# Kernel tuning notes

Hardware: AMD Instinct MI355X
Metric: run time of the kernel (lower is better)

## Reference

```python
import jax, jax.numpy as jnp
import numpy as np

HIDDEN = 32
ODE_H = 0.1      # rk4 fixed step size (torchdiffeq options step_size=0.1)
ODE_STEPS = 10   # integrate t in [0, 1]


def gcn_conv(x, W, b, edge_index, n):
    """PyG GCNConv: symmetric norm with self-loops; x' = D^-1/2 (A+I) D^-1/2 (x W) + b."""
    h = x @ W                                  # [n, out]
    src, dst = edge_index[0], edge_index[1]
    deg = jnp.ones((n,), h.dtype).at[dst].add(1.0)   # +1 for self-loop
    dinv = jax.lax.rsqrt(deg)
    coef = (dinv[src] * dinv[dst])[:, None]
    agg = jnp.zeros_like(h).at[dst].add(h[src] * coef)
    agg = agg + h * (dinv * dinv)[:, None]     # self-loop term
    return agg + b


def ode_rk4(x0, edge_index, Wg, bg, wt, n):
    """RK4 integration of psi(t,x)=relu(GCN(x)) * sigmoid(t * wt) from t=0 to 1."""
    def f(t, x):
        gate = jax.nn.sigmoid(t * wt)          # [hidden], Linear(1,h,no bias).sigmoid()
        return jax.nn.relu(gcn_conv(x, Wg, bg, edge_index, n)) * gate

    h = ODE_H
    def step(x, t):
        k1 = f(t, x)
        k2 = f(t + h * 0.5, x + (h * 0.5) * k1)
        k3 = f(t + h * 0.5, x + (h * 0.5) * k2)
        k4 = f(t + h, x + h * k3)
        return x + (h / 6.0) * (k1 + 2.0 * k2 + 2.0 * k3 + k4), None

    ts = jnp.arange(ODE_STEPS, dtype=x0.dtype) * h
    xf, _ = jax.lax.scan(step, x0, ts)
    return xf


def setup_inputs() -> dict:
    key = jax.random.key(0)
    ks = jax.random.split(key, 16)
    N, IN, H = 100000, 128, HIDDEN
    E, DE = 1600000, 800000

    inp = {
        "H_t": jax.random.normal(ks[0], (N, IN), jnp.float32),
        "A_pos_t": jax.random.randint(ks[1], (2, E), 0, N),
        "A_neg_t": jax.random.randint(ks[2], (2, E), 0, N),
        "dA_pos": jax.random.randint(ks[3], (2, DE), 0, N),
        "dA_neg": jax.random.randint(ks[4], (2, DE), 0, N),
        # init GCN
        "W_init": jax.random.normal(ks[5], (IN, H), jnp.float32) / np.sqrt(IN),
        "b_init": jnp.zeros((H,), jnp.float32),
        # pos ODE func
        "W_pos": jax.random.normal(ks[6], (H, H), jnp.float32) / np.sqrt(H),
        "b_pos": jnp.zeros((H,), jnp.float32),
        "wt_pos": jax.random.normal(ks[7], (H,), jnp.float32),
        # neg ODE func
        "W_neg": jax.random.normal(ks[8], (H, H), jnp.float32) / np.sqrt(H),
        "b_neg": jnp.zeros((H,), jnp.float32),
        "wt_neg": jax.random.normal(ks[9], (H,), jnp.float32),
        # combine + layernorm
        "W_comb": jax.random.normal(ks[10], (2 * H, H), jnp.float32) / np.sqrt(2 * H),
        "b_comb": jnp.zeros((H,), jnp.float32),
        "ln_g": jnp.ones((H,), jnp.float32),
        "ln_b": jnp.zeros((H,), jnp.float32),
    }
    return inp


def reference(H_t, A_pos_t, A_neg_t, dA_pos, dA_neg,
              W_init, b_init, W_pos, b_pos, wt_pos,
              W_neg, b_neg, wt_neg, W_comb, b_comb, ln_g, ln_b):
    n = H_t.shape[0]
    edges_all = jnp.concatenate([A_pos_t, A_neg_t], axis=1)
    H = jax.nn.relu(gcn_conv(H_t, W_init, b_init, edges_all, n))   # [n, hidden]
    Z_pos = ode_rk4(H, dA_pos, W_pos, b_pos, wt_pos, n)
    Z_neg = ode_rk4(H, dA_neg, W_neg, b_neg, wt_neg, n)
    Z = jnp.concatenate([Z_pos, Z_neg], axis=-1) @ W_comb + b_comb # [n, hidden]
    mu = jnp.mean(Z, axis=-1, keepdims=True)
    var = jnp.var(Z, axis=-1, keepdims=True)
    return (Z - mu) * jax.lax.rsqrt(var + 1e-5) * ln_g + ln_b
```

## Files before the change

kernel.cpp:

```cpp
#include <hip/hip_runtime.h>
#include <math.h>


#define TPB 256
#define SCAN_T 1024

typedef _Float16 h8 __attribute__((ext_vector_type(8)));
typedef float f8 __attribute__((ext_vector_type(8)));


struct SegG { const int* src; const int* dst; int n; int goff; };
struct FSeg { const int* src; const int* dst; int n; const int* offs; int* cur; };

__global__ __launch_bounds__(TPB) void count_mm(
        SegG s0, SegG s1, SegG s2, SegG s3, int* __restrict__ cnt3,
        unsigned short* __restrict__ rank,
        const float* __restrict__ x, const float* __restrict__ W,
        _Float16* __restrict__ hs, int N, int cntB, int mmB) {
    __shared__ float Ws[128][32];
    __shared__ float xs[8][128];

    int g5 = blockIdx.x / 5, r5 = blockIdx.x % 5;
    if (r5 < 3) {
        int cb = g5 * 3 + r5;
        if (cb >= cntB) return;
        int i = cb * TPB + threadIdx.x;
        SegG s; int e;
        if (i < s0.n) { s = s0; e = i; }
        else if (i < s0.n + s1.n) { s = s1; e = i - s0.n; }
        else if (i < s0.n + s1.n + s2.n) { s = s2; e = i - s0.n - s1.n; }
        else if (i < s0.n + s1.n + s2.n + s3.n) { s = s3; e = i - s0.n - s1.n - s2.n; }
        else return;
        int r = atomicAdd(&cnt3[s.goff + s.dst[e]], 1);
        if (rank) rank[i] = (unsigned short)r;
    } else {
        int mb = g5 * 2 + (r5 - 3);
        if (mb >= mmB) return;
        int tid = threadIdx.x;
        for (int i = tid; i < 128 * 32; i += TPB) Ws[i >> 5][i & 31] = W[i];
        int base = mb * 8;
        for (int i = tid; i < 8 * 128; i += TPB) {
            int idx = base * 128 + i;
            xs[i >> 7][i & 127] = (idx < N * 128) ? x[idx] : 0.0f;
        }
        __syncthreads();
        int row = tid >> 5, c = tid & 31;
        int gr = base + row;
        float acc = 0.0f;
#pragma unroll
        for (int k = 0; k < 128; ++k) acc += xs[row][k] * Ws[k][c];
        if (gr < N) hs[gr * 32 + c] = (_Float16)acc;
    }
}

__global__ void fill4_rank(SegG s0, SegG s1, SegG s2, SegG s3,
                           const int* __restrict__ offs3,
                           const unsigned short* __restrict__ rank,
                           int* __restrict__ csr) {
    int i = blockIdx.x * blockDim.x + threadIdx.x;
    SegG s; int e;
    if (i < s0.n) { s = s0; e = i; }
    else if (i < s0.n + s1.n) { s = s1; e = i - s0.n; }
    else if (i < s0.n + s1.n + s2.n) { s = s2; e = i - s0.n - s1.n; }
    else if (i < s0.n + s1.n + s2.n + s3.n) { s = s3; e = i - s0.n - s1.n - s2.n; }
    else return;
    csr[offs3[s.goff + s.dst[e]] + (int)rank[i]] = s.src[e];
}

__global__ void fill4(FSeg s0, FSeg s1, FSeg s2, FSeg s3, int* __restrict__ csr) {
    int i = blockIdx.x * blockDim.x + threadIdx.x;
    FSeg s; int e;
    if (i < s0.n) { s = s0; e = i; }
    else if (i < s0.n + s1.n) { s = s1; e = i - s0.n; }
    else if (i < s0.n + s1.n + s2.n) { s = s2; e = i - s0.n - s1.n; }
    else if (i < s0.n + s1.n + s2.n + s3.n) { s = s3; e = i - s0.n - s1.n - s2.n; }
    else return;
    int d = s.dst[e];
    int pos = s.offs[d] + atomicAdd(&s.cur[d], 1);
    csr[pos] = s.src[e];
}

__global__ void scan_block(const int* __restrict__ in, int n, int* __restrict__ out,
                           int* __restrict__ bsums, float* __restrict__ dinv) {
    __shared__ int sh[SCAN_T];
    int tx = threadIdx.x;
    int g = blockIdx.x * SCAN_T + tx;
    int v = (g < n) ? in[g] : 0;
    if (g < n) dinv[g] = rsqrtf(1.0f + (float)v);
    sh[tx] = v;
    __syncthreads();
    for (int off = 1; off < SCAN_T; off <<= 1) {
        int t = (tx >= off) ? sh[tx - off] : 0;
        __syncthreads();
        sh[tx] += t;
        __syncthreads();
    }
    if (g < n) out[g] = sh[tx] - v;
    if (tx == SCAN_T - 1) bsums[blockIdx.x] = sh[tx];
}

__global__ void scan_sums(int* __restrict__ bsums, int nb) {
    __shared__ int sh[SCAN_T];
    int tx = threadIdx.x;
    int v = (tx < nb) ? bsums[tx] : 0;
    sh[tx] = v;
    __syncthreads();
    for (int off = 1; off < SCAN_T; off <<= 1) {
        int t = (tx >= off) ? sh[tx - off] : 0;
        __syncthreads();
        sh[tx] += t;
        __syncthreads();
    }
    if (tx < nb) bsums[tx] = sh[tx] - v;
}

__global__ void scan_add(int* __restrict__ offs, const int* __restrict__ bsums, int n, int total) {
    int g = blockIdx.x * blockDim.x + threadIdx.x;
    if (g < n) offs[g] += bsums[g >> 10];
    if (g == 0) offs[n] = total;
}


__global__ void mm32_kernel(const float* __restrict__ x, const float* __restrict__ W,
                            const float* __restrict__ dinv, _Float16* __restrict__ hs, int N) {
    __shared__ float Ws[32][32];
    __shared__ float xs[8][32];
    int tid = threadIdx.x;
    for (int i = tid; i < 32 * 32; i += TPB) Ws[i >> 5][i & 31] = W[i];
    int base = blockIdx.x * 8;
    {
        int idx = base * 32 + tid;
        xs[tid >> 5][tid & 31] = (idx < N * 32) ? x[idx] : 0.0f;
    }
    __syncthreads();
    int row = tid >> 5, c = tid & 31;
    int gr = base + row;
    float acc = 0.0f;
#pragma unroll
    for (int k = 0; k < 32; ++k) acc += xs[row][k] * Ws[k][c];
    if (gr < N) hs[gr * 32 + c] = (_Float16)(acc * dinv[gr]);
}


struct Job {
    const int* offs; const int* csr;
    const _Float16* hs_in; _Float16* hs_out;
    const float* dinv; const float* dinv_next;
    const float* bias; const float* wt;
    _Float16* ksum; float* x;
    const float* W;
    const float* sdinv;
};

__global__ __launch_bounds__(TPB) void agg_stage(Job jp, Job jn, int nbg, float t,
                                                 int stage, int do_mm, int split,
                                                 float* __restrict__ x2, int N) {
    __shared__ float Ws[32][32];
    __shared__ float xts[64][36];
    __shared__ int soffs[65];

    bool isP; int bid;
    if (split) {
        int xcd = blockIdx.x & 7;
        isP = xcd < 4;
        bid = ((int)blockIdx.x >> 3) * 4 + (xcd & 3);
        if (bid >= nbg) return;
    } else {
        isP = (int)blockIdx.x < nbg;
        bid = isP ? blockIdx.x : (blockIdx.x - nbg);
    }
    const Job& J = isP ? jp : jn;
    int nbase = bid * 64;
    int tid = threadIdx.x;
    int lnode = tid >> 2, q = tid & 3;
    int node = nbase + lnode;
    bool valid = node < N;

    if (do_mm) {
        for (int i = tid; i < 32 * 32; i += TPB) Ws[i >> 5][i & 31] = J.W[i];
    }
    if (tid < 65) {
        int ix = nbase + tid; if (ix > N) ix = N;
        soffs[tid] = J.offs[ix];
    }
    __syncthreads();

    f8 xrow;
#pragma unroll
    for (int j = 0; j < 8; ++j) xrow[j] = 0.f;

    if (valid) {
        const h8* hsv = (const h8*)J.hs_in;
        const int* __restrict__ csr = J.csr;
        int r0 = soffs[lnode], r1 = soffs[lnode + 1];
        f8 acc;
        if (J.sdinv) {
            const float* __restrict__ sd = J.sdinv;
            acc = __builtin_convertvector(hsv[node * 4 + q], f8) * sd[node];
            int i = r0;
            for (; i + 4 <= r1; i += 4) {
                int e0 = csr[i], e1 = csr[i + 1], e2 = csr[i + 2], e3 = csr[i + 3];
                float d0 = sd[e0], d1 = sd[e1], d2 = sd[e2], d3 = sd[e3];
                h8 v0 = hsv[e0 * 4 + q];
                h8 v1 = hsv[e1 * 4 + q];
                h8 v2 = hsv[e2 * 4 + q];
                h8 v3 = hsv[e3 * 4 + q];
                acc += __builtin_convertvector(v0, f8) * d0
                     + __builtin_convertvector(v1, f8) * d1
                     + __builtin_convertvector(v2, f8) * d2
                     + __builtin_convertvector(v3, f8) * d3;
            }
            for (; i < r1; ++i) {
                int e = csr[i];
                acc += __builtin_convertvector(hsv[e * 4 + q], f8) * sd[e];
            }
        } else {
            acc = __builtin_convertvector(hsv[node * 4 + q], f8);
            int i = r0;
            for (; i + 4 <= r1; i += 4) {
                int e0 = csr[i], e1 = csr[i + 1], e2 = csr[i + 2], e3 = csr[i + 3];
                h8 v0 = hsv[e0 * 4 + q];
                h8 v1 = hsv[e1 * 4 + q];
                h8 v2 = hsv[e2 * 4 + q];
                h8 v3 = hsv[e3 * 4 + q];
                acc += (__builtin_convertvector(v0, f8) + __builtin_convertvector(v1, f8))
                     + (__builtin_convertvector(v2, f8) + __builtin_convertvector(v3, f8));
            }
            for (; i < r1; ++i)
                acc += __builtin_convertvector(hsv[csr[i] * 4 + q], f8);
        }

        float dv = J.dinv[node];
        f8 bb = ((const f8*)J.bias)[q];
        f8 kv;
#pragma unroll
        for (int j = 0; j < 8; ++j) kv[j] = fmaxf(acc[j] * dv + bb[j], 0.f);
        if (J.wt) {
            f8 w = ((const f8*)J.wt)[q];
#pragma unroll
            for (int j = 0; j < 8; ++j) kv[j] *= 1.f / (1.f + expf(-t * w[j]));
        }
        int idx = node * 4 + q;
        f8* x8 = (f8*)J.x;
        h8* ks8 = (h8*)J.ksum;
        if (stage == 0) {
            x8[idx] = kv;
            ((f8*)x2)[idx] = kv;
            xrow = kv;
        } else if (stage == 4) {
            f8 ks = __builtin_convertvector(ks8[idx], f8);
            f8 xv = x8[idx];
            const float cc = 0.1f / 6.0f;
#pragma unroll
            for (int j = 0; j < 8; ++j) xv[j] += cc * (ks[j] + kv[j]);
            x8[idx] = xv;
            xrow = xv;
        } else {
            float a = (stage == 3) ? 0.1f : 0.05f;
            f8 xv = x8[idx];
#pragma unroll
            for (int j = 0; j < 8; ++j) xrow[j] = xv[j] + a * kv[j];
            if (stage == 1) {
                ks8[idx] = __builtin_convertvector(kv, h8);
            } else {
                f8 ks = __builtin_convertvector(ks8[idx], f8);
#pragma unroll
                for (int j = 0; j < 8; ++j) ks[j] += 2.f * kv[j];
                ks8[idx] = __builtin_convertvector(ks, h8);
            }
        }
    }

    if (do_mm) {
        if (valid) {
#pragma unroll
            for (int j = 0; j < 8; ++j) xts[lnode][q * 8 + j] = xrow[j];
        }
        __syncthreads();
        if (valid) {
            f8 accm;
#pragma unroll
            for (int j = 0; j < 8; ++j) accm[j] = 0.f;
#pragma unroll
            for (int k = 0; k < 32; ++k) {
                float xv = xts[lnode][k];
                f8 w = *(const f8*)&Ws[k][q * 8];
                accm += xv * w;
            }
            accm *= J.dinv_next[node];
            ((h8*)J.hs_out)[node * 4 + q] = __builtin_convertvector(accm, h8);
        }
    }
}


__global__ void combine_kernel(const float* __restrict__ zp, const float* __restrict__ zn,
                               const float* __restrict__ Wc, const float* __restrict__ bc,
                               const float* __restrict__ g, const float* __restrict__ be,
                               float* __restrict__ out, int N) {
    __shared__ float Ws[64][32];
    __shared__ float zs[8][64];
    int tid = threadIdx.x;
    for (int i = tid; i < 64 * 32; i += TPB) Ws[i >> 5][i & 31] = Wc[i];
    int base = blockIdx.x * 8;
    {
        int r = tid >> 5, c = tid & 31;
        int gr = base + r;
        zs[r][c] = (gr < N) ? zp[gr * 32 + c] : 0.0f;
        zs[r][32 + c] = (gr < N) ? zn[gr * 32 + c] : 0.0f;
    }
    __syncthreads();
    int row = tid >> 5, c = tid & 31;
    int gr = base + row;
    float acc = bc[c];
#pragma unroll
    for (int k = 0; k < 64; ++k) acc += zs[row][k] * Ws[k][c];
    float s = acc, sq = acc * acc;
#pragma unroll
    for (int off = 16; off; off >>= 1) {
        s += __shfl_xor(s, off, 32);
        sq += __shfl_xor(sq, off, 32);
    }
    float mu = s * (1.0f / 32.0f);
    float var = sq * (1.0f / 32.0f) - mu * mu;
    float y = (acc - mu) * rsqrtf(var + 1e-5f) * g[c] + be[c];
    if (gr < N) out[gr * 32 + c] = y;
}


extern "C" void kernel_launch(void* const* d_in, const int* in_sizes, int n_in,
                              void* d_out, int out_size, void* d_ws, size_t ws_size,
                              hipStream_t stream) {
    const float* H_t = (const float*)d_in[0];
    const int* Apos = (const int*)d_in[1];
    const int* Aneg = (const int*)d_in[2];
    const int* dApos = (const int*)d_in[3];
    const int* dAneg = (const int*)d_in[4];
    const float* W_init = (const float*)d_in[5];
    const float* b_init = (const float*)d_in[6];
    const float* W_pos = (const float*)d_in[7];
    const float* b_pos = (const float*)d_in[8];
    const float* wt_pos = (const float*)d_in[9];
    const float* W_neg = (const float*)d_in[10];
    const float* b_neg = (const float*)d_in[11];
    const float* wt_neg = (const float*)d_in[12];
    const float* W_comb = (const float*)d_in[13];
    const float* b_comb = (const float*)d_in[14];
    const float* ln_g = (const float*)d_in[15];
    const float* ln_b = (const float*)d_in[16];

    const int N = in_sizes[0] / 128;
    const int E1 = in_sizes[1] / 2;
    const int E2 = in_sizes[2] / 2;
    const int DE1 = in_sizes[3] / 2;
    const int DE2 = in_sizes[4] / 2;
    const int Etot = E1 + E2 + DE1 + DE2;
    const int n3 = 3 * N;

    const int* Apos_src = Apos, * Apos_dst = Apos + E1;
    const int* Aneg_src = Aneg, * Aneg_dst = Aneg + E2;
    const int* dApos_src = dApos, * dApos_dst = dApos + DE1;
    const int* dAneg_src = dAneg, * dAneg_dst = dAneg + DE2;

    const size_t n32 = (size_t)N * 32;
    const size_t szf = n32 * 4;
    const size_t szh = n32 * 2;
    auto al = [](size_t b) { return (b + 255) & ~(size_t)255; };

    size_t small_bytes = 3 * al((size_t)n3 * 4)
                       + al(((size_t)n3 + 1) * 4)
                       + al((size_t)Etot * 4)
                       + al(SCAN_T * 4);
    size_t need_merged = 2 * al(szf) + 6 * al(szh) + small_bytes;
    size_t need_rank = need_merged + al((size_t)Etot * 2);
    bool merged = ws_size >= need_merged + 4096;
    bool use_rank = ws_size >= need_rank + 4096;

    char* p = (char*)d_ws;
    auto alloc = [&](size_t bytes) -> void* {
        void* r = (void*)p;
        p += al(bytes);
        return r;
    };
    float* x_pos = (float*)alloc(szf);
    float* x_neg = (float*)alloc(szf);
    _Float16* ksum_p = (_Float16*)alloc(szh);
    _Float16* ksum_n = merged ? (_Float16*)alloc(szh) : ksum_p;
    _Float16* hs_pa = (_Float16*)alloc(szh);
    _Float16* hs_pb = (_Float16*)alloc(szh);
    _Float16* hs_na = merged ? (_Float16*)alloc(szh) : hs_pa;
    _Float16* hs_nb = merged ? (_Float16*)alloc(szh) : hs_pb;
    float* dinv3 = (float*)alloc((size_t)n3 * 4);
    int* cnt3 = (int*)alloc((size_t)n3 * 4);
    int* cur3 = (int*)alloc((size_t)n3 * 4);
    int* offs3 = (int*)alloc(((size_t)n3 + 1) * 4);
    int* csr3 = (int*)alloc((size_t)Etot * 4);
    int* bsums = (int*)alloc(SCAN_T * 4);
    unsigned short* rank = use_rank ? (unsigned short*)alloc((size_t)Etot * 2) : nullptr;

    hipMemsetAsync(cnt3, 0, 2 * al((size_t)n3 * 4), stream);

    float* dinv_all = dinv3, * dinv_pos = dinv3 + N, * dinv_neg = dinv3 + 2 * N;
    const int* offs_all = offs3, * offs_pos = offs3 + N, * offs_neg = offs3 + 2 * N;

    dim3 blk(TPB);
    auto gblk = [](int n) { return dim3((n + TPB - 1) / TPB); };
    dim3 grid_rows((N + 7) / 8);
    const int nb64 = (N + 63) / 64;
    const int nbs = (n3 + SCAN_T - 1) / SCAN_T;
    const int nsplit = ((nb64 + 3) / 4) * 8;

    SegG s0 = { Apos_src, Apos_dst, E1, 0 };
    SegG s1 = { Aneg_src, Aneg_dst, E2, 0 };
    SegG s2 = { dApos_src, dApos_dst, DE1, N };
    SegG s3 = { dAneg_src, dAneg_dst, DE2, 2 * N };
    {
        const int cntB = (Etot + TPB - 1) / TPB;
        const int mmB = (N + 7) / 8;
        const int g5 = max((cntB + 2) / 3, (mmB + 1) / 2);
        count_mm<<<dim3(5 * g5), blk, 0, stream>>>(s0, s1, s2, s3, cnt3, rank,
                                                   H_t, W_init, hs_pa, N, cntB, mmB);
    }
    scan_block<<<nbs, SCAN_T, 0, stream>>>(cnt3, n3, offs3, bsums, dinv3);
    scan_sums<<<1, SCAN_T, 0, stream>>>(bsums, nbs);
    scan_add<<<gblk(n3), blk, 0, stream>>>(offs3, bsums, n3, Etot);
    if (use_rank) {
        fill4_rank<<<gblk(Etot), blk, 0, stream>>>(s0, s1, s2, s3, offs3, rank, csr3);
    } else {
        FSeg f0 = { Apos_src, Apos_dst, E1, offs3, cur3 };
        FSeg f1 = { Aneg_src, Aneg_dst, E2, offs3, cur3 };
        FSeg f2 = { dApos_src, dApos_dst, DE1, offs3 + N, cur3 + N };
        FSeg f3 = { dAneg_src, dAneg_dst, DE2, offs3 + 2 * N, cur3 + 2 * N };
        fill4<<<gblk(Etot), blk, 0, stream>>>(f0, f1, f2, f3, csr3);
    }

    auto mkjob = [&](const int* offs, const _Float16* hs_in, _Float16* hs_out,
                     const float* dinv, const float* dinv_next, const float* bias,
                     const float* wt, _Float16* ksum, float* x, const float* W,
                     const float* sdinv) {
        Job j; j.offs = offs; j.csr = csr3; j.hs_in = hs_in; j.hs_out = hs_out;
        j.dinv = dinv; j.dinv_next = dinv_next; j.bias = bias; j.wt = wt;
        j.ksum = ksum; j.x = x; j.W = W; j.sdinv = sdinv; return j;
    };

    {
        Job j0 = mkjob(offs_all, hs_pa, hs_pb, dinv_all, dinv_pos, b_init,
                       nullptr, nullptr, x_pos, W_pos, dinv_all);
        agg_stage<<<nb64, blk, 0, stream>>>(j0, j0, nb64, 0.0f, 0, 1, 0, x_neg, N);
    }

    if (merged) {
        mm32_kernel<<<grid_rows, blk, 0, stream>>>(x_neg, W_neg, dinv_neg, hs_nb, N);
        for (int s = 0; s < 10; ++s) {
            float t0 = 0.1f * (float)s;
            int last_mm = (s == 9) ? 0 : 1;
            Job p1 = mkjob(offs_pos, hs_pb, hs_pa, dinv_pos, dinv_pos, b_pos, wt_pos, ksum_p, x_pos, W_pos, nullptr);
            Job n1 = mkjob(offs_neg, hs_nb, hs_na, dinv_neg, dinv_neg, b_neg, wt_neg, ksum_n, x_neg, W_neg, nullptr);
            agg_stage<<<nsplit, blk, 0, stream>>>(p1, n1, nb64, t0, 1, 1, 1, nullptr, N);
            Job p2 = p1; p2.hs_in = hs_pa; p2.hs_out = hs_pb;
            Job n2 = n1; n2.hs_in = hs_na; n2.hs_out = hs_nb;
            agg_stage<<<nsplit, blk, 0, stream>>>(p2, n2, nb64, t0 + 0.05f, 2, 1, 1, nullptr, N);
            agg_stage<<<nsplit, blk, 0, stream>>>(p1, n1, nb64, t0 + 0.05f, 3, 1, 1, nullptr, N);
            agg_stage<<<nsplit, blk, 0, stream>>>(p2, n2, nb64, t0 + 0.1f, 4, last_mm, 1, nullptr, N);
        }
    } else {
        for (int ode = 0; ode < 2; ++ode) {
            float* x = ode ? x_neg : x_pos;
            const float* W = ode ? W_neg : W_pos;
            const float* b = ode ? b_neg : b_pos;
            const float* wt = ode ? wt_neg : wt_pos;
            const float* dinv = ode ? dinv_neg : dinv_pos;
            const int* offs = ode ? offs_neg : offs_pos;
            if (ode == 1) {
                mm32_kernel<<<grid_rows, blk, 0, stream>>>(x, W, dinv, hs_pb, N);
            }
            for (int s = 0; s < 10; ++s) {
                float t0 = 0.1f * (float)s;
                int last_mm = (s == 9) ? 0 : 1;
                Job j1 = mkjob(offs, hs_pb, hs_pa, dinv, dinv, b, wt, ksum_p, x, W, nullptr);
                Job j2 = j1; j2.hs_in = hs_pa; j2.hs_out = hs_pb;
                agg_stage<<<nb64, blk, 0, stream>>>(j1, j1, nb64, t0, 1, 1, 0, nullptr, N);
                agg_stage<<<nb64, blk, 0, stream>>>(j2, j2, nb64, t0 + 0.05f, 2, 1, 0, nullptr, N);
                agg_stage<<<nb64, blk, 0, stream>>>(j1, j1, nb64, t0 + 0.05f, 3, 1, 0, nullptr, N);
                agg_stage<<<nb64, blk, 0, stream>>>(j2, j2, nb64, t0 + 0.1f, 4, last_mm, 0, nullptr, N);
            }
        }
    }

    combine_kernel<<<grid_rows, blk, 0, stream>>>(x_pos, x_neg, W_comb, b_comb, ln_g, ln_b,
                                                  (float*)d_out, N);
}
```

Before: 2.023 ms.

## Fuse pre-scaling, neg-ODE matmul, last RK4 stage and combine kernels

The initial matmul now writes fp32 to a temp buffer, and a new combined fill/scale kernel multiplies each row by dinv and converts it to fp16. This removes the per-edge dinv gather in the initial aggregation. The init aggregation also computes the neg-ODE projection (W2) in the same pass, so the separate mm32 launch goes away. The final RK4 stage is fused with the combine matmul and layernorm, and the scan_sums plus scan_add pair is replaced by a single kernel that does a serial prefix sum of the block sums in shared memory. These changes cut launches and memory passes but add extra fp32 temp traffic and a serial per-thread prefix loop.

Result: faster. 1.954 ms (-3.4%).

```diff
diff --git a/kernel.cpp b/kernel.cpp
--- a/kernel.cpp
+++ b/kernel.cpp
@@ -16,7 +16,7 @@
         SegG s0, SegG s1, SegG s2, SegG s3, int* __restrict__ cnt3,
         unsigned short* __restrict__ rank,
         const float* __restrict__ x, const float* __restrict__ W,
-        _Float16* __restrict__ hs, int N, int cntB, int mmB) {
+        float* __restrict__ temp, int N, int cntB, int mmB) {
     __shared__ float Ws[128][32];
     __shared__ float xs[8][128];
 
@@ -49,22 +49,45 @@
         float acc = 0.0f;
 #pragma unroll
         for (int k = 0; k < 128; ++k) acc += xs[row][k] * Ws[k][c];
-        if (gr < N) hs[gr * 32 + c] = (_Float16)acc;
-    }
-}
-
-__global__ void fill4_rank(SegG s0, SegG s1, SegG s2, SegG s3,
-                           const int* __restrict__ offs3,
-                           const unsigned short* __restrict__ rank,
-                           int* __restrict__ csr) {
-    int i = blockIdx.x * blockDim.x + threadIdx.x;
-    SegG s; int e;
-    if (i < s0.n) { s = s0; e = i; }
-    else if (i < s0.n + s1.n) { s = s1; e = i - s0.n; }
-    else if (i < s0.n + s1.n + s2.n) { s = s2; e = i - s0.n - s1.n; }
-    else if (i < s0.n + s1.n + s2.n + s3.n) { s = s3; e = i - s0.n - s1.n - s2.n; }
-    else return;
-    csr[offs3[s.goff + s.dst[e]] + (int)rank[i]] = s.src[e];
+        if (gr < N) temp[gr * 32 + c] = acc;
+    }
+}
+
+__global__ __launch_bounds__(TPB) void fill_scale(
+        SegG s0, SegG s1, SegG s2, SegG s3,
+        const int* __restrict__ offs3, const unsigned short* __restrict__ rank,
+        int* __restrict__ csr,
+        const float* __restrict__ temp, const float* __restrict__ dinv,
+        _Float16* __restrict__ hs, int N, int fillB, int scaleB) {
+    int g13 = blockIdx.x / 13, r13 = blockIdx.x % 13;
+    if (r13 < 12) {
+        int fb = g13 * 12 + r13;
+        if (fb >= fillB) return;
+        int i = fb * TPB + threadIdx.x;
+        SegG s; int e;
+        if (i < s0.n) { s = s0; e = i; }
+        else if (i < s0.n + s1.n) { s = s1; e = i - s0.n; }
+        else if (i < s0.n + s1.n + s2.n) { s = s2; e = i - s0.n - s1.n; }
+        else if (i < s0.n + s1.n + s2.n + s3.n) { s = s3; e = i - s0.n - s1.n - s2.n; }
+        else return;
+        csr[offs3[s.goff + s.dst[e]] + (int)rank[i]] = s.src[e];
+    } else {
+        int c = g13 * TPB + threadIdx.x;
+        if (c < N * 4) {
+            f8 v = ((const f8*)temp)[c];
+            float dv = dinv[c >> 2];
+            ((h8*)hs)[c] = __builtin_convertvector(v * dv, h8);
+        }
+    }
+}
+
+__global__ void scale_hs(const float* __restrict__ temp, const float* __restrict__ dinv,
+                         _Float16* __restrict__ hs, int N) {
+    int c = blockIdx.x * blockDim.x + threadIdx.x;
+    if (c < N * 4) {
+        f8 v = ((const f8*)temp)[c];
+        ((h8*)hs)[c] = __builtin_convertvector(v * dinv[c >> 2], h8);
+    }
 }
 
 __global__ void fill4(FSeg s0, FSeg s1, FSeg s2, FSeg s3, int* __restrict__ csr) {
@@ -120,6 +143,22 @@
     if (g == 0) offs[n] = total;
 }
 
+__global__ void scan_add2(int* __restrict__ offs, const int* __restrict__ bsums,
+                          int n, int total, int nbs) {
+    __shared__ int sb[SCAN_T];
+    int tid = threadIdx.x;
+    for (int i = tid; i < nbs; i += TPB) sb[i] = bsums[i];
+    __syncthreads();
+    int g = blockIdx.x * TPB + tid;
+    if (g < n) {
+        int b = g >> 10;
+        int pre = 0;
+        for (int j = 0; j < b; ++j) pre += sb[j];
+        offs[g] += pre;
+    }
+    if (g == 0) offs[n] = total;
+}
+
 
 __global__ void mm32_kernel(const float* __restrict__ x, const float* __restrict__ W,
                             const float* __restrict__ dinv, _Float16* __restrict__ hs, int N) {
@@ -149,13 +188,14 @@
     const float* bias; const float* wt;
     _Float16* ksum; float* x;
     const float* W;
-    const float* sdinv;
+    const float* W2; const float* dinv2; _Float16* hs_out2;
 };
 
 __global__ __launch_bounds__(TPB) void agg_stage(Job jp, Job jn, int nbg, float t,
                                                  int stage, int do_mm, int split,
                                                  float* __restrict__ x2, int N) {
     __shared__ float Ws[32][32];
+    __shared__ float Ws2[32][32];
     __shared__ float xts[64][36];
     __shared__ int soffs[65];
 
@@ -178,6 +218,9 @@
 
     if (do_mm) {
         for (int i = tid; i < 32 * 32; i += TPB) Ws[i >> 5][i & 31] = J.W[i];
+        if (J.W2) {
+            for (int i = tid; i < 32 * 32; i += TPB) Ws2[i >> 5][i & 31] = J.W2[i];
+        }
     }
     if (tid < 65) {
         int ix = nbase + tid; if (ix > N) ix = N;
@@ -193,29 +236,125 @@
         const h8* hsv = (const h8*)J.hs_in;
         const int* __restrict__ csr = J.csr;
         int r0 = soffs[lnode], r1 = soffs[lnode + 1];
-        f8 acc;
-        if (J.sdinv) {
-            const float* __restrict__ sd = J.sdinv;
-            acc = __builtin_convertvector(hsv[node * 4 + q], f8) * sd[node];
-            int i = r0;
-            for (; i + 4 <= r1; i += 4) {
-                int e0 = csr[i], e1 = csr[i + 1], e2 = csr[i + 2], e3 = csr[i + 3];
-                float d0 = sd[e0], d1 = sd[e1], d2 = sd[e2], d3 = sd[e3];
-                h8 v0 = hsv[e0 * 4 + q];
-                h8 v1 = hsv[e1 * 4 + q];
-                h8 v2 = hsv[e2 * 4 + q];
-                h8 v3 = hsv[e3 * 4 + q];
-                acc += __builtin_convertvector(v0, f8) * d0
-                     + __builtin_convertvector(v1, f8) * d1
-                     + __builtin_convertvector(v2, f8) * d2
-                     + __builtin_convertvector(v3, f8) * d3;
+        f8 acc = __builtin_convertvector(hsv[node * 4 + q], f8);
+        int i = r0;
+        for (; i + 4 <= r1; i += 4) {
+            int e0 = csr[i], e1 = csr[i + 1], e2 = csr[i + 2], e3 = csr[i + 3];
+            h8 v0 = hsv[e0 * 4 + q];
+            h8 v1 = hsv[e1 * 4 + q];
+            h8 v2 = hsv[e2 * 4 + q];
+            h8 v3 = hsv[e3 * 4 + q];
+            acc += (__builtin_convertvector(v0, f8) + __builtin_convertvector(v1, f8))
+                 + (__builtin_convertvector(v2, f8) + __builtin_convertvector(v3, f8));
+        }
+        for (; i < r1; ++i)
+            acc += __builtin_convertvector(hsv[csr[i] * 4 + q], f8);
+
+        float dv = J.dinv[node];
+        f8 bb = ((const f8*)J.bias)[q];
+        f8 kv;
+#pragma unroll
+        for (int j = 0; j < 8; ++j) kv[j] = fmaxf(acc[j] * dv + bb[j], 0.f);
+        if (J.wt) {
+            f8 w = ((const f8*)J.wt)[q];
+#pragma unroll
+            for (int j = 0; j < 8; ++j) kv[j] *= 1.f / (1.f + expf(-t * w[j]));
+        }
+        int idx = node * 4 + q;
+        f8* x8 = (f8*)J.x;
+        h8* ks8 = (h8*)J.ksum;
+        if (stage == 0) {
+            x8[idx] = kv;
+            ((f8*)x2)[idx] = kv;
+            xrow = kv;
+        } else if (stage == 4) {
+            f8 ks = __builtin_convertvector(ks8[idx], f8);
+            f8 xv = x8[idx];
+            const float cc = 0.1f / 6.0f;
+#pragma unroll
+            for (int j = 0; j < 8; ++j) xv[j] += cc * (ks[j] + kv[j]);
+            x8[idx] = xv;
+            xrow = xv;
+        } else {
+            float a = (stage == 3) ? 0.1f : 0.05f;
+            f8 xv = x8[idx];
+#pragma unroll
+            for (int j = 0; j < 8; ++j) xrow[j] = xv[j] + a * kv[j];
+            if (stage == 1) {
+                ks8[idx] = __builtin_convertvector(kv, h8);
+            } else {
+                f8 ks = __builtin_convertvector(ks8[idx], f8);
+#pragma unroll
+                for (int j = 0; j < 8; ++j) ks[j] += 2.f * kv[j];
+                ks8[idx] = __builtin_convertvector(ks, h8);
             }
-            for (; i < r1; ++i) {
-                int e = csr[i];
-                acc += __builtin_convertvector(hsv[e * 4 + q], f8) * sd[e];
+        }
+    }
+
+    if (do_mm) {
+        if (valid) {
+#pragma unroll
+            for (int j = 0; j < 8; ++j) xts[lnode][q * 8 + j] = xrow[j];
+        }
+        __syncthreads();
+        if (valid) {
+            f8 accm;
+#pragma unroll
+            for (int j = 0; j < 8; ++j) accm[j] = 0.f;
+#pragma unroll
+            for (int k = 0; k < 32; ++k) {
+                float xv = xts[lnode][k];
+                f8 w = *(const f8*)&Ws[k][q * 8];
+                accm += xv * w;
             }
-        } else {
-            acc = __builtin_convertvector(hsv[node * 4 + q], f8);
+            accm *= J.dinv_next[node];
+            ((h8*)J.hs_out)[node * 4 + q] = __builtin_convertvector(accm, h8);
+            if (J.W2) {
+                f8 acc2;
+#pragma unroll
+                for (int j = 0; j < 8; ++j) acc2[j] = 0.f;
+#pragma unroll
+                for (int k = 0; k < 32; ++k) {
+                    float xv = xts[lnode][k];
+                    f8 w = *(const f8*)&Ws2[k][q * 8];
+                    acc2 += xv * w;
+                }
+                acc2 *= J.dinv2[node];
+                ((h8*)J.hs_out2)[node * 4 + q] = __builtin_convertvector(acc2, h8);
+            }
+        }
+    }
+}
+
+__global__ __launch_bounds__(TPB) void stage4_combine(
+        Job jp, Job jn, float t,
+        const float* __restrict__ Wc, const float* __restrict__ bc,
+        const float* __restrict__ lg, const float* __restrict__ lb,
+        float* __restrict__ out, int N) {
+    __shared__ float Ws[64][32];
+    __shared__ float xts[64][68];
+    __shared__ int soffs[65];
+
+    int tid = threadIdx.x;
+    for (int i = tid; i < 64 * 32; i += TPB) Ws[i >> 5][i & 31] = Wc[i];
+    int nbase = blockIdx.x * 64;
+    int lnode = tid >> 2, q = tid & 3;
+    int node = nbase + lnode;
+    bool valid = node < N;
+
+    for (int side = 0; side < 2; ++side) {
+        const Job& J = side ? jn : jp;
+        __syncthreads();
+        if (tid < 65) {
+            int ix = nbase + tid; if (ix > N) ix = N;
+            soffs[tid] = J.offs[ix];
+        }
+        __syncthreads();
+        if (valid) {
+            const h8* hsv = (const h8*)J.hs_in;
+            const int* __restrict__ csr = J.csr;
+            int r0 = soffs[lnode], r1 = soffs[lnode + 1];
+            f8 acc = __builtin_convertvector(hsv[node * 4 + q], f8);
             int i = r0;
             for (; i + 4 <= r1; i += 4) {
                 int e0 = csr[i], e1 = csr[i + 1], e2 = csr[i + 2], e3 = csr[i + 3];
@@ -228,68 +367,52 @@
             }
             for (; i < r1; ++i)
                 acc += __builtin_convertvector(hsv[csr[i] * 4 + q], f8);
-        }
-
-        float dv = J.dinv[node];
-        f8 bb = ((const f8*)J.bias)[q];
-        f8 kv;
-#pragma unroll
-        for (int j = 0; j < 8; ++j) kv[j] = fmaxf(acc[j] * dv + bb[j], 0.f);
-        if (J.wt) {
+
+            float dv = J.dinv[node];
+            f8 bb = ((const f8*)J.bias)[q];
+            f8 kv;
+#pragma unroll
+            for (int j = 0; j < 8; ++j) kv[j] = fmaxf(acc[j] * dv + bb[j], 0.f);
             f8 w = ((const f8*)J.wt)[q];
 #pragma unroll
             for (int j = 0; j < 8; ++j) kv[j] *= 1.f / (1.f + expf(-t * w[j]));
-        }
-        int idx = node * 4 + q;
-        f8* x8 = (f8*)J.x;
-        h8* ks8 = (h8*)J.ksum;
-        if (stage == 0) {
-            x8[idx] = kv;
-            ((f8*)x2)[idx] = kv;
-            xrow = kv;
-        } else if (stage == 4) {
-            f8 ks = __builtin_convertvector(ks8[idx], f8);
-            f8 xv = x8[idx];
+
+            int idx = node * 4 + q;
+            f8 ks = __builtin_convertvector(((const h8*)J.ksum)[idx], f8);
+            f8 xv = ((const f8*)J.x)[idx];
             const float cc = 0.1f / 6.0f;
 #pragma unroll
-            for (int j = 0; j < 8; ++j) xv[j] += cc * (ks[j] + kv[j]);
-            x8[idx] = xv;
-            xrow = xv;
-        } else {
-            float a = (stage == 3) ? 0.1f : 0.05f;
-            f8 xv = x8[idx];
-#pragma unroll
-            for (int j = 0; j < 8; ++j) xrow[j] = xv[j] + a * kv[j];
-            if (stage == 1) {
-                ks8[idx] = __builtin_convertvector(kv, h8);
-            } else {
-                f8 ks = __builtin_convertvector(ks8[idx], f8);
-#pragma unroll
-                for (int j = 0; j < 8; ++j) ks[j] += 2.f * kv[j];
-                ks8[idx] = __builtin_convertvector(ks, h8);
-            }
-        }
-    }
-
-    if (do_mm) {
-        if (valid) {
-#pragma unroll
-            for (int j = 0; j < 8; ++j) xts[lnode][q * 8 + j] = xrow[j];
-        }
-        __syncthreads();
-        if (valid) {
-            f8 accm;
-#pragma unroll
-            for (int j = 0; j < 8; ++j) accm[j] = 0.f;
-#pragma unroll
-            for (int k = 0; k < 32; ++k) {
-                float xv = xts[lnode][k];
-                f8 w = *(const f8*)&Ws[k][q * 8];
-                accm += xv * w;
-            }
-            accm *= J.dinv_next[node];
-            ((h8*)J.hs_out)[node * 4 + q] = __builtin_convertvector(accm, h8);
-        }
+            for (int j = 0; j < 8; ++j)
+                xts[lnode][side * 32 + q * 8 + j] = xv[j] + cc * (ks[j] + kv[j]);
+        }
+    }
+    __syncthreads();
+
+    if (valid) {
+        f8 bcv = ((const f8*)bc)[q];
+        f8 accm;
+#pragma unroll
+        for (int j = 0; j < 8; ++j) accm[j] = bcv[j];
+#pragma unroll
+        for (int k = 0; k < 64; ++k) {
+            float xv = xts[lnode][k];
+            f8 w = *(const f8*)&Ws[k][q * 8];
+            accm += xv * w;
+        }
+        float s = 0.f, sq = 0.f;
+#pragma unroll
+        for (int j = 0; j < 8; ++j) { s += accm[j]; sq += accm[j] * accm[j]; }
+        s += __shfl_xor(s, 1); s += __shfl_xor(s, 2);
+        sq += __shfl_xor(sq, 1); sq += __shfl_xor(sq, 2);
+        float mu = s * (1.0f / 32.0f);
+        float var = sq * (1.0f / 32.0f) - mu * mu;
+        float rs = rsqrtf(var + 1e-5f);
+        f8 gv = ((const f8*)lg)[q];
+        f8 bv = ((const f8*)lb)[q];
+        f8 o;
+#pragma unroll
+        for (int j = 0; j < 8; ++j) o[j] = (accm[j] - mu) * rs * gv[j] + bv[j];
+        ((f8*)out)[node * 4 + q] = o;
     }
 }
 
@@ -414,19 +537,27 @@
     SegG s1 = { Aneg_src, Aneg_dst, E2, 0 };
     SegG s2 = { dApos_src, dApos_dst, DE1, N };
     SegG s3 = { dAneg_src, dAneg_dst, DE2, 2 * N };
+    const int cntB = (Etot + TPB - 1) / TPB;
+    const int mmB = (N + 7) / 8;
     {
-        const int cntB = (Etot + TPB - 1) / TPB;
-        const int mmB = (N + 7) / 8;
         const int g5 = max((cntB + 2) / 3, (mmB + 1) / 2);
         count_mm<<<dim3(5 * g5), blk, 0, stream>>>(s0, s1, s2, s3, cnt3, rank,
-                                                   H_t, W_init, hs_pa, N, cntB, mmB);
+                                                   H_t, W_init, x_pos, N, cntB, mmB);
     }
     scan_block<<<nbs, SCAN_T, 0, stream>>>(cnt3, n3, offs3, bsums, dinv3);
-    scan_sums<<<1, SCAN_T, 0, stream>>>(bsums, nbs);
-    scan_add<<<gblk(n3), blk, 0, stream>>>(offs3, bsums, n3, Etot);
+    if (nbs <= SCAN_T / 4 * 4 && nbs <= 1024) {
+        scan_add2<<<gblk(n3), blk, 0, stream>>>(offs3, bsums, n3, Etot, nbs);
+    } else {
+        scan_sums<<<1, SCAN_T, 0, stream>>>(bsums, nbs);
+        scan_add<<<gblk(n3), blk, 0, stream>>>(offs3, bsums, n3, Etot);
+    }
+    const int scaleB = (N * 4 + TPB - 1) / TPB;
     if (use_rank) {
-        fill4_rank<<<gblk(Etot), blk, 0, stream>>>(s0, s1, s2, s3, offs3, rank, csr3);
+        const int g13 = max((cntB + 11) / 12, scaleB);
+        fill_scale<<<dim3(13 * g13), blk, 0, stream>>>(s0, s1, s2, s3, offs3, rank, csr3,
+                                                       x_pos, dinv_all, hs_pa, N, cntB, scaleB);
     } else {
+        scale_hs<<<gblk(N * 4), blk, 0, stream>>>(x_pos, dinv_all, hs_pa, N);
         FSeg f0 = { Apos_src, Apos_dst, E1, offs3, cur3 };
         FSeg f1 = { Aneg_src, Aneg_dst, E2, offs3, cur3 };
         FSeg f2 = { dApos_src, dApos_dst, DE1, offs3 + N, cur3 + N };
@@ -436,32 +567,37 @@
 
     auto mkjob = [&](const int* offs, const _Float16* hs_in, _Float16* hs_out,
                      const float* dinv, const float* dinv_next, const float* bias,
-                     const float* wt, _Float16* ksum, float* x, const float* W,
-                     const float* sdinv) {
+                     const float* wt, _Float16* ksum, float* x, const float* W) {
         Job j; j.offs = offs; j.csr = csr3; j.hs_in = hs_in; j.hs_out = hs_out;
         j.dinv = dinv; j.dinv_next = dinv_next; j.bias = bias; j.wt = wt;
-        j.ksum = ksum; j.x = x; j.W = W; j.sdinv = sdinv; return j;
+        j.ksum = ksum; j.x = x; j.W = W;
+        j.W2 = nullptr; j.dinv2 = nullptr; j.hs_out2 = nullptr; return j;
     };
 
     {
         Job j0 = mkjob(offs_all, hs_pa, hs_pb, dinv_all, dinv_pos, b_init,
-                       nullptr, nullptr, x_pos, W_pos, dinv_all);
+                       nullptr, nullptr, x_pos, W_pos);
+        if (merged) { j0.W2 = W_neg; j0.dinv2 = dinv_neg; j0.hs_out2 = hs_nb; }
         agg_stage<<<nb64, blk, 0, stream>>>(j0, j0, nb64, 0.0f, 0, 1, 0, x_neg, N);
     }
 
     if (merged) {
-        mm32_kernel<<<grid_rows, blk, 0, stream>>>(x_neg, W_neg, dinv_neg, hs_nb, N);
         for (int s = 0; s < 10; ++s) {
             float t0 = 0.1f * (float)s;
-            int last_mm = (s == 9) ? 0 : 1;
-            Job p1 = mkjob(offs_pos, hs_pb, hs_pa, dinv_pos, dinv_pos, b_pos, wt_pos, ksum_p, x_pos, W_pos, nullptr);
-            Job n1 = mkjob(offs_neg, hs_nb, hs_na, dinv_neg, dinv_neg, b_neg, wt_neg, ksum_n, x_neg, W_neg, nullptr);
+            Job p1 = mkjob(offs_pos, hs_pb, hs_pa, dinv_pos, dinv_pos, b_pos, wt_pos, ksum_p, x_pos, W_pos);
+            Job n1 = mkjob(offs_neg, hs_nb, hs_na, dinv_neg, dinv_neg, b_neg, wt_neg, ksum_n, x_neg, W_neg);
             agg_stage<<<nsplit, blk, 0, stream>>>(p1, n1, nb64, t0, 1, 1, 1, nullptr, N);
             Job p2 = p1; p2.hs_in = hs_pa; p2.hs_out = hs_pb;
             Job n2 = n1; n2.hs_in = hs_na; n2.hs_out = hs_nb;
             agg_stage<<<nsplit, blk, 0, stream>>>(p2, n2, nb64, t0 + 0.05f, 2, 1, 1, nullptr, N);
             agg_stage<<<nsplit, blk, 0, stream>>>(p1, n1, nb64, t0 + 0.05f, 3, 1, 1, nullptr, N);
-            agg_stage<<<nsplit, blk, 0, stream>>>(p2, n2, nb64, t0 + 0.1f, 4, last_mm, 1, nullptr, N);
+            if (s < 9) {
+                agg_stage<<<nsplit, blk, 0, stream>>>(p2, n2, nb64, t0 + 0.1f, 4, 1, 1, nullptr, N);
+            } else {
+                stage4_combine<<<nb64, blk, 0, stream>>>(p2, n2, t0 + 0.1f,
+                                                         W_comb, b_comb, ln_g, ln_b,
+                                                         (float*)d_out, N);
+            }
         }
     } else {
         for (int ode = 0; ode < 2; ++ode) {
@@ -477,7 +613,7 @@
             for (int s = 0; s < 10; ++s) {
                 float t0 = 0.1f * (float)s;
                 int last_mm = (s == 9) ? 0 : 1;
-                Job j1 = mkjob(offs, hs_pb, hs_pa, dinv, dinv, b, wt, ksum_p, x, W, nullptr);
+                Job j1 = mkjob(offs, hs_pb, hs_pa, dinv, dinv, b, wt, ksum_p, x, W);
                 Job j2 = j1; j2.hs_in = hs_pa; j2.hs_out = hs_pb;
                 agg_stage<<<nb64, blk, 0, stream>>>(j1, j1, nb64, t0, 1, 1, 0, nullptr, N);
                 agg_stage<<<nb64, blk, 0, stream>>>(j2, j2, nb64, t0 + 0.05f, 2, 1, 0, nullptr, N);
@@ -485,8 +621,7 @@
                 agg_stage<<<nb64, blk, 0, stream>>>(j2, j2, nb64, t0 + 0.1f, 4, last_mm, 0, nullptr, N);
             }
         }
-    }
-
-    combine_kernel<<<grid_rows, blk, 0, stream>>>(x_pos, x_neg, W_comb, b_comb, ln_g, ln_b,
-                                                  (float*)d_out, N);
-}
+        combine_kernel<<<grid_rows, blk, 0, stream>>>(x_pos, x_neg, W_comb, b_comb, ln_g, ln_b,
+                                                      (float*)d_out, N);
+    }
+}
```
